# Performance work log

Measured on AMD Instinct MI355X. Metric: run time of the kernel, lower is better.

Reference implementation:

```python
import jax, jax.numpy as jnp
import numpy as np

N, E = 50000, 800000
IN_DIM, HID, HEADS, OUT_DIM = 128, 64, 4, 64
NEG_SLOPE = 0.2


def add_self_loops(edge_index, n):
    loops = jnp.arange(n, dtype=edge_index.dtype)
    return jnp.concatenate([edge_index, jnp.stack([loops, loops])], axis=1)


def gat_layer(x, edge_index, W, att_src, att_dst, bias, heads, ch, concat):
    n = x.shape[0]
    xp = (x @ W).reshape(n, heads, ch)                       # [N,H,C]
    s_src = jnp.sum(xp * att_src, axis=-1)                   # [N,H]
    s_dst = jnp.sum(xp * att_dst, axis=-1)                   # [N,H]
    src, dst = edge_index[0], edge_index[1]
    e = jax.nn.leaky_relu(s_src[src] + s_dst[dst], NEG_SLOPE)  # [E,H]
    # segment softmax over incoming edges of each destination node
    m = jax.ops.segment_max(e, dst, num_segments=n)
    e = jnp.exp(e - m[dst])
    denom = jax.ops.segment_sum(e, dst, num_segments=n)
    alpha = e / (denom[dst] + 1e-16)                         # [E,H]
    out = jax.ops.segment_sum(xp[src] * alpha[:, :, None], dst, num_segments=n)  # [N,H,C]
    out = out.reshape(n, heads * ch) if concat else out.mean(axis=1)
    return out + bias


def setup_inputs() -> dict:
    key = jax.random.key(0)
    ks = jax.random.split(key, 10)
    glorot = lambda k, shape: jax.random.normal(k, shape, jnp.float32) * np.sqrt(2.0 / (shape[0] + shape[-1]))
    return {
        "x": jax.random.normal(ks[0], (N, IN_DIM), jnp.float32),
        "edge_index": jax.random.randint(ks[1], (2, E), 0, N, jnp.int32),
        "W1": glorot(ks[2], (IN_DIM, HEADS * HID)),
        "att_src1": glorot(ks[3], (HEADS, HID)),
        "att_dst1": glorot(ks[4], (HEADS, HID)),
        "bias1": jnp.zeros((HEADS * HID,), jnp.float32),
        "W2": glorot(ks[5], (HEADS * HID, OUT_DIM)),
        "att_src2": glorot(ks[6], (1, OUT_DIM)),
        "att_dst2": glorot(ks[7], (1, OUT_DIM)),
        "bias2": jnp.zeros((OUT_DIM,), jnp.float32),
    }


def reference(x, edge_index, W1, att_src1, att_dst1, bias1, W2, att_src2, att_dst2, bias2):
    ei = add_self_loops(edge_index, x.shape[0])
    h = gat_layer(x, ei, W1, att_src1, att_dst1, bias1, HEADS, HID, concat=True)
    h = jax.nn.relu(h)
    out = gat_layer(h, ei, W2, att_src2, att_dst2, bias2, 1, OUT_DIM, concat=False)
    return out
```

## Files before the change

### kernel.cpp

```cpp
#include <hip/hip_runtime.h>
#include <hip/hip_bf16.h>
#include <hip/hip_fp16.h>

#define NODES 50000
#define NEDGE 800000
#define NE2   850000
#define INDIM 128
#define F1    256
#define HEADS 4
#define HID   64
#define OUTD  64
#define MTILES 3125

#define NB   196
#define PB   196
#define EPB  4096
#define CAP  6144
#define G1B  782

typedef _Float16 f16;
typedef _Float16 f16x8 __attribute__((ext_vector_type(8)));
typedef float    f32x4 __attribute__((ext_vector_type(4)));

__global__ void k_hist(const int* __restrict__ ei, int* __restrict__ blkhist,
                       const float* __restrict__ W1, const float* __restrict__ W2,
                       f16* __restrict__ W1p, f16* __restrict__ W2p)
{
    const int b = blockIdx.x, t = threadIdx.x;
    if (b < PB) {
        __shared__ int h[NB];
        for (int i = t; i < NB; i += 256) h[i] = 0;
        __syncthreads();
        const int e0 = b * EPB;
        const int eend = min(e0 + EPB, NEDGE);
        for (int i = e0 + t; i < eend; i += 256) {
            int d = ei[NEDGE + i];
            atomicAdd(&h[d >> 8], 1);
        }
        __syncthreads();
        for (int i = t; i < NB; i += 256) blkhist[i * PB + b] = h[i];
    } else {
        int idx = (b - PB) * 256 + t;
        if (idx < 32768) {
            int j = idx & 7, l = (idx >> 3) & 63, fi = idx >> 9;
            int kb = fi & 3, ct = fi >> 2;
            int k = kb * 32 + (l >> 4) * 8 + j;
            int col = ct * 16 + (l & 15);
            W1p[idx] = (f16)W1[k * F1 + col];
        } else {
            int i2 = idx - 32768;
            int j = i2 & 7, l = (i2 >> 3) & 63, fi = i2 >> 9;
            int kb = fi & 7, ct = fi >> 3;
            int k = kb * 32 + (l >> 4) * 8 + j;
            int col = ct * 16 + (l & 15);
            W2p[i2] = (f16)W2[k * OUTD + col];
        }
    }
}

__global__ void k_scanR(int* __restrict__ blkhist, int* __restrict__ rowtot)
{
    __shared__ int sh[256];
    const int q = blockIdx.x, t = threadIdx.x;
    int v = (t < PB) ? blkhist[q * PB + t] : 0;
    sh[t] = v; __syncthreads();
    for (int off = 1; off < 256; off <<= 1) {
        int tv = (t >= off) ? sh[t - off] : 0;
        __syncthreads();
        sh[t] += tv;
        __syncthreads();
    }
    if (t < PB) blkhist[q * PB + t] = sh[t] - v;
    if (t == 255) rowtot[q] = sh[255];
}

__global__ void k_part(const int* __restrict__ ei, const int* __restrict__ blkhist,
                       const int* __restrict__ rowtot, unsigned* __restrict__ staged)
{
    const int b = blockIdx.x, t = threadIdx.x;
    __shared__ int sS[256];
    __shared__ int cur[NB];
    int v = (t < NB) ? rowtot[t] : 0;
    sS[t] = v; __syncthreads();
    for (int off = 1; off < 256; off <<= 1) {
        int tv = (t >= off) ? sS[t - off] : 0;
        __syncthreads();
        sS[t] += tv;
        __syncthreads();
    }
    if (t < NB) cur[t] = (sS[t] - v) + blkhist[t * PB + b];
    __syncthreads();
    const int e0 = b * EPB;
    const int eend = min(e0 + EPB, NEDGE);
    for (int i = e0 + t; i < eend; i += 256) {
        int sN = ei[i];
        int d  = ei[NEDGE + i];
        int pos = atomicAdd(&cur[d >> 8], 1);
        staged[pos] = (unsigned)sN | ((unsigned)(d & 255) << 16);
    }
}

__global__ __launch_bounds__(256) void k_bg(
    const unsigned* __restrict__ staged, const int* __restrict__ rowtot,
    int* __restrict__ row_ptr, int* __restrict__ csr_src,
    const float* __restrict__ x, const f16* __restrict__ W1p,
    const float* __restrict__ as1, const float* __restrict__ ad1,
    f16* __restrict__ xp1h, float* __restrict__ ssrc, float* __restrict__ sdst)
{
    if (blockIdx.x < NB) {
        __shared__ unsigned sorted2[CAP];
        __shared__ int bin[256];
        __shared__ int cnt[256];
        __shared__ int sh[256];
        __shared__ int ssum[4];
        const int q = blockIdx.x, t = threadIdx.x;
        const int wv = t >> 6, lane = t & 63;
        int pv = (t < q) ? rowtot[t] : 0;
#pragma unroll
        for (int off = 32; off; off >>= 1) pv += __shfl_xor(pv, off);
        if (lane == 0) ssum[wv] = pv;
        cnt[t] = 0; bin[t] = 0;
        __syncthreads();
        const int estart = ssum[0] + ssum[1] + ssum[2] + ssum[3];
        const int m = rowtot[q];
        const int nodebase = q * 256;
        const int nn = min(256, NODES - nodebase);
        const int csrbase = estart + nodebase;

        const bool dosort = (m <= CAP);
        if (dosort) {
            for (int i = t; i < m; i += 256)
                atomicAdd(&bin[(staged[estart + i] & 0xFFFFu) >> 8], 1);
            __syncthreads();
            int bv = bin[t];
            sh[t] = bv;
            __syncthreads();
            for (int off = 1; off < 256; off <<= 1) {
                int tv = (t >= off) ? sh[t - off] : 0;
                __syncthreads();
                sh[t] += tv;
                __syncthreads();
            }
            bin[t] = sh[t] - bv;
            __syncthreads();
            for (int i = t; i < m; i += 256) {
                unsigned u = staged[estart + i];
                int p = atomicAdd(&bin[(u & 0xFFFFu) >> 8], 1);
                sorted2[p] = u;
            }
            __syncthreads();
        }

        if (dosort) {
            for (int i = t; i < m; i += 256)
                atomicAdd(&cnt[sorted2[i] >> 16], 1);
        } else {
            for (int i = t; i < m; i += 256)
                atomicAdd(&cnt[staged[estart + i] >> 16], 1);
        }
        __syncthreads();
        int v = cnt[t];
        sh[t] = v;
        __syncthreads();
        for (int off = 1; off < 256; off <<= 1) {
            int tv = (t >= off) ? sh[t - off] : 0;
            __syncthreads();
            sh[t] += tv;
            __syncthreads();
        }
        int excl = sh[t] - v;
        __syncthreads();
        if (t < nn) {
            int r = csrbase + excl + t;
            row_ptr[nodebase + t] = r;
            csr_src[r] = nodebase + t;
            cnt[t] = excl + t + 1;
        }
        __syncthreads();
        if (dosort) {
            for (int i = t; i < m; i += 256) {
                unsigned u = sorted2[i];
                int pos = atomicAdd(&cnt[u >> 16], 1);
                csr_src[csrbase + pos] = (int)(u & 0xFFFFu);
            }
        } else {
            for (int i = t; i < m; i += 256) {
                unsigned u = staged[estart + i];
                int pos = atomicAdd(&cnt[u >> 16], 1);
                csr_src[csrbase + pos] = (int)(u & 0xFFFFu);
            }
        }
        if (q == NB - 1 && t == 0) row_ptr[NODES] = NE2;
        return;
    }

    const int wv = threadIdx.x >> 6, lane = threadIdx.x & 63;
    const int l15 = lane & 15, quad = lane >> 4;
    const int rowtile = (blockIdx.x - NB) * 4 + wv;
    if (rowtile >= MTILES) return;
    const int rowbase = rowtile * 16;

    f16x8 afrag[4];
    const float* xrow = x + (rowbase + l15) * INDIM + quad * 8;
#pragma unroll
    for (int kb = 0; kb < 4; ++kb) {
        float4 u0 = *(const float4*)(xrow + kb * 32);
        float4 u1 = *(const float4*)(xrow + kb * 32 + 4);
        f16x8 a;
        a[0] = (f16)u0.x; a[1] = (f16)u0.y; a[2] = (f16)u0.z; a[3] = (f16)u0.w;
        a[4] = (f16)u1.x; a[5] = (f16)u1.y; a[6] = (f16)u1.z; a[7] = (f16)u1.w;
        afrag[kb] = a;
    }

    const f16x8* Wf = (const f16x8*)W1p;
    f32x4 acc[16];
#pragma unroll
    for (int ct = 0; ct < 16; ++ct) acc[ct] = (f32x4){0.f, 0.f, 0.f, 0.f};
#pragma unroll
    for (int ct = 0; ct < 16; ++ct) {
#pragma unroll
        for (int kb = 0; kb < 4; ++kb) {
            f16x8 b = Wf[(ct * 4 + kb) * 64 + lane];
            acc[ct] = __builtin_amdgcn_mfma_f32_16x16x32_f16(afrag[kb], b, acc[ct], 0, 0, 0);
        }
    }
    const int orow = rowbase + quad * 4;
#pragma unroll
    for (int ct = 0; ct < 16; ++ct) {
#pragma unroll
        for (int r = 0; r < 4; ++r)
            xp1h[(orow + r) * F1 + ct * 16 + l15] = (f16)acc[ct][r];
    }
    float ps[4][4], pd[4][4];
#pragma unroll
    for (int h = 0; h < 4; ++h)
#pragma unroll
        for (int r = 0; r < 4; ++r) { ps[h][r] = 0.f; pd[h][r] = 0.f; }
#pragma unroll
    for (int ct = 0; ct < 16; ++ct) {
        float av = as1[ct * 16 + l15];
        float dv = ad1[ct * 16 + l15];
        int h = ct >> 2;
#pragma unroll
        for (int r = 0; r < 4; ++r) {
            ps[h][r] = fmaf(acc[ct][r], av, ps[h][r]);
            pd[h][r] = fmaf(acc[ct][r], dv, pd[h][r]);
        }
    }
#pragma unroll
    for (int off = 8; off; off >>= 1) {
#pragma unroll
        for (int h = 0; h < 4; ++h)
#pragma unroll
            for (int r = 0; r < 4; ++r) {
                ps[h][r] += __shfl_xor(ps[h][r], off);
                pd[h][r] += __shfl_xor(pd[h][r], off);
            }
    }
    if (l15 == 0) {
#pragma unroll
        for (int r = 0; r < 4; ++r) {
            int row = orow + r;
            float4 vs = {ps[0][r], ps[1][r], ps[2][r], ps[3][r]};
            float4 vd = {pd[0][r], pd[1][r], pd[2][r], pd[3][r]};
            ((float4*)ssrc)[row] = vs;
            ((float4*)sdst)[row] = vd;
        }
    }
}

__global__ __launch_bounds__(256) void k_agg1(
    const int* __restrict__ row_ptr, const int* __restrict__ csr_src,
    const float* __restrict__ ssrc, const float* __restrict__ sdst,
    const f16* __restrict__ xp1h, const float* __restrict__ bias,
    f16* __restrict__ hbuf)
{
    const int wv = threadIdx.x >> 6, l = threadIdx.x & 63;
    const int n = blockIdx.x * 4 + wv;
    const int eq = l & 15, ph = l >> 4;
    const int g  = l >> 4, sub = l & 15;
    const int sel_lo = (sub >> 3) << 4;
    const int sel_hi = (2 + (sub >> 3)) << 4;
    const float sd = sdst[n * HEADS + ph];
    const int jbeg = row_ptr[n], jend = row_ptr[n + 1];
    const f16x8* xv = (const f16x8*)xp1h;

    float den = 0.f;
    float alo[8] = {0.f,0.f,0.f,0.f,0.f,0.f,0.f,0.f};
    float ahi[8] = {0.f,0.f,0.f,0.f,0.f,0.f,0.f,0.f};
    for (int base = jbeg; base < jend; base += 16) {
        int c = jend - base; if (c > 16) c = 16;
        int s = 0; float ex = 0.f;
        if (eq < c) {
            s = csr_src[base + eq];
            float e = ssrc[s * HEADS + ph] + sd;
            e = e > 0.f ? e : 0.2f * e;
            ex = __expf(e);
        }
        den += ex;
        int p = 0;
        for (; p + 7 < c; p += 8) {
            int ea = p + g, eb = p + 4 + g;
            int   sa  = __shfl(s, ea),          sb  = __shfl(s, eb);
            float aal = __shfl(ex, ea | sel_lo), aah = __shfl(ex, ea | sel_hi);
            float abl = __shfl(ex, eb | sel_lo), abh = __shfl(ex, eb | sel_hi);
            f16x8 va0 = xv[sa * 32 + sub];
            f16x8 va1 = xv[sa * 32 + sub + 16];
            f16x8 vb0 = xv[sb * 32 + sub];
            f16x8 vb1 = xv[sb * 32 + sub + 16];
#pragma unroll
            for (int j = 0; j < 8; ++j) {
                alo[j] = fmaf(aal, (float)va0[j], alo[j]);
                ahi[j] = fmaf(aah, (float)va1[j], ahi[j]);
            }
#pragma unroll
            for (int j = 0; j < 8; ++j) {
                alo[j] = fmaf(abl, (float)vb0[j], alo[j]);
                ahi[j] = fmaf(abh, (float)vb1[j], ahi[j]);
            }
        }
        for (; p < c; p += 4) {
            int ea = p + g;
            int   sa  = __shfl(s, ea);
            float aal = __shfl(ex, ea | sel_lo), aah = __shfl(ex, ea | sel_hi);
            f16x8 va0 = xv[sa * 32 + sub];
            f16x8 va1 = xv[sa * 32 + sub + 16];
#pragma unroll
            for (int j = 0; j < 8; ++j) {
                alo[j] = fmaf(aal, (float)va0[j], alo[j]);
                ahi[j] = fmaf(aah, (float)va1[j], ahi[j]);
            }
        }
    }
#pragma unroll
    for (int off = 8; off; off >>= 1) den += __shfl_xor(den, off);
    const float dl = __shfl(den, sel_lo);
    const float dh = __shfl(den, sel_hi);
    const float rdl = 1.f / (dl + 1e-16f);
    const float rdh = 1.f / (dh + 1e-16f);
#pragma unroll
    for (int j = 0; j < 8; ++j) {
        alo[j] += __shfl_xor(alo[j], 16); alo[j] += __shfl_xor(alo[j], 32);
        ahi[j] += __shfl_xor(ahi[j], 16); ahi[j] += __shfl_xor(ahi[j], 32);
    }
    if (g == 0) {
        const float4* b4 = (const float4*)bias;
        float4 bl0 = b4[sub * 2],        bl1 = b4[sub * 2 + 1];
        float4 bh0 = b4[(sub + 16) * 2], bh1 = b4[(sub + 16) * 2 + 1];
        f16x8 olo, ohi;
        float v;
        v = fmaf(alo[0], rdl, bl0.x); olo[0] = (f16)(v > 0.f ? v : 0.f);
        v = fmaf(alo[1], rdl, bl0.y); olo[1] = (f16)(v > 0.f ? v : 0.f);
        v = fmaf(alo[2], rdl, bl0.z); olo[2] = (f16)(v > 0.f ? v : 0.f);
        v = fmaf(alo[3], rdl, bl0.w); olo[3] = (f16)(v > 0.f ? v : 0.f);
        v = fmaf(alo[4], rdl, bl1.x); olo[4] = (f16)(v > 0.f ? v : 0.f);
        v = fmaf(alo[5], rdl, bl1.y); olo[5] = (f16)(v > 0.f ? v : 0.f);
        v = fmaf(alo[6], rdl, bl1.z); olo[6] = (f16)(v > 0.f ? v : 0.f);
        v = fmaf(alo[7], rdl, bl1.w); olo[7] = (f16)(v > 0.f ? v : 0.f);
        v = fmaf(ahi[0], rdh, bh0.x); ohi[0] = (f16)(v > 0.f ? v : 0.f);
        v = fmaf(ahi[1], rdh, bh0.y); ohi[1] = (f16)(v > 0.f ? v : 0.f);
        v = fmaf(ahi[2], rdh, bh0.z); ohi[2] = (f16)(v > 0.f ? v : 0.f);
        v = fmaf(ahi[3], rdh, bh0.w); ohi[3] = (f16)(v > 0.f ? v : 0.f);
        v = fmaf(ahi[4], rdh, bh1.x); ohi[4] = (f16)(v > 0.f ? v : 0.f);
        v = fmaf(ahi[5], rdh, bh1.y); ohi[5] = (f16)(v > 0.f ? v : 0.f);
        v = fmaf(ahi[6], rdh, bh1.z); ohi[6] = (f16)(v > 0.f ? v : 0.f);
        v = fmaf(ahi[7], rdh, bh1.w); ohi[7] = (f16)(v > 0.f ? v : 0.f);
        ((f16x8*)hbuf)[n * 32 + sub] = olo;
        ((f16x8*)hbuf)[n * 32 + sub + 16] = ohi;
    }
}

__global__ __launch_bounds__(256) void k_gemm2m(
    const f16* __restrict__ hbuf, const f16* __restrict__ W2p,
    const float* __restrict__ as2, const float* __restrict__ ad2,
    f16* __restrict__ xp2h, float* __restrict__ ssrc, float* __restrict__ sdst)
{
    const int wv = threadIdx.x >> 6, lane = threadIdx.x & 63;
    const int l15 = lane & 15, quad = lane >> 4;
    const int rowtile = blockIdx.x * 4 + wv;
    if (rowtile >= MTILES) return;
    const int rowbase = rowtile * 16;

    const f16x8* Wf = (const f16x8*)W2p;
    f32x4 acc[4];
#pragma unroll
    for (int ct = 0; ct < 4; ++ct) acc[ct] = (f32x4){0.f, 0.f, 0.f, 0.f};
    const f16* hrow = hbuf + (rowbase + l15) * F1 + quad * 8;
#pragma unroll
    for (int kb = 0; kb < 8; ++kb) {
        f16x8 a = *(const f16x8*)(hrow + kb * 32);
#pragma unroll
        for (int ct = 0; ct < 4; ++ct) {
            f16x8 b = Wf[(ct * 8 + kb) * 64 + lane];
            acc[ct] = __builtin_amdgcn_mfma_f32_16x16x32_f16(a, b, acc[ct], 0, 0, 0);
        }
    }
    const int orow = rowbase + quad * 4;
#pragma unroll
    for (int ct = 0; ct < 4; ++ct) {
#pragma unroll
        for (int r = 0; r < 4; ++r)
            xp2h[(orow + r) * OUTD + ct * 16 + l15] = (f16)acc[ct][r];
    }
    float ps[4] = {0.f,0.f,0.f,0.f}, pd[4] = {0.f,0.f,0.f,0.f};
#pragma unroll
    for (int ct = 0; ct < 4; ++ct) {
        float av = as2[ct * 16 + l15];
        float dv = ad2[ct * 16 + l15];
#pragma unroll
        for (int r = 0; r < 4; ++r) {
            ps[r] = fmaf(acc[ct][r], av, ps[r]);
            pd[r] = fmaf(acc[ct][r], dv, pd[r]);
        }
    }
#pragma unroll
    for (int off = 8; off; off >>= 1) {
#pragma unroll
        for (int r = 0; r < 4; ++r) {
            ps[r] += __shfl_xor(ps[r], off);
            pd[r] += __shfl_xor(pd[r], off);
        }
    }
    if (l15 == 0) {
#pragma unroll
        for (int r = 0; r < 4; ++r) {
            ssrc[orow + r] = ps[r];
            sdst[orow + r] = pd[r];
        }
    }
}

__global__ __launch_bounds__(256) void k_agg2(
    const int* __restrict__ row_ptr, const int* __restrict__ csr_src,
    const float* __restrict__ ssrc, const float* __restrict__ sdst,
    const f16* __restrict__ xp2h, const float* __restrict__ bias,
    float* __restrict__ out)
{
    const int wv = threadIdx.x >> 6, l = threadIdx.x & 63;
    const int n = blockIdx.x * 4 + wv;
    const int grp = l >> 3, sub = l & 7;
    const float sd = sdst[n];
    const int jbeg = row_ptr[n], jend = row_ptr[n + 1];
    const f16x8* xv = (const f16x8*)xp2h;

    float den = 0.f;
    float acc[8] = {0.f,0.f,0.f,0.f,0.f,0.f,0.f,0.f};
    for (int base = jbeg; base < jend; base += 64) {
        int c = jend - base; if (c > 64) c = 64;
        int s = 0; float ex = 0.f;
        if (l < c) {
            s = csr_src[base + l];
            float e = ssrc[s] + sd;
            e = e > 0.f ? e : 0.2f * e;
            ex = __expf(e);
        }
        den += ex;
        int i = 0;
        for (; 8 * (i + 1) < c; i += 2) {
            int ea = 8 * i + grp, eb = 8 * i + 8 + grp;
            int   sa = __shfl(s, ea),  sb = __shfl(s, eb);
            float aa = __shfl(ex, ea), ab = __shfl(ex, eb);
            f16x8 va = xv[sa * 8 + sub];
            f16x8 vb = xv[sb * 8 + sub];
#pragma unroll
            for (int j = 0; j < 8; ++j) acc[j] = fmaf(aa, (float)va[j], acc[j]);
#pragma unroll
            for (int j = 0; j < 8; ++j) acc[j] = fmaf(ab, (float)vb[j], acc[j]);
        }
        for (; 8 * i < c; ++i) {
            int eidx = 8 * i + grp;
            int   se = __shfl(s, eidx);
            float ae = __shfl(ex, eidx);
            f16x8 v = xv[se * 8 + sub];
#pragma unroll
            for (int j = 0; j < 8; ++j) acc[j] = fmaf(ae, (float)v[j], acc[j]);
        }
    }
#pragma unroll
    for (int off = 32; off; off >>= 1) den += __shfl_xor(den, off);
    const float rd = 1.f / (den + 1e-16f);
#pragma unroll
    for (int j = 0; j < 8; ++j) {
        acc[j] += __shfl_xor(acc[j], 8);
        acc[j] += __shfl_xor(acc[j], 16);
        acc[j] += __shfl_xor(acc[j], 32);
    }
    if (grp == 0) {
        const float4* b4 = (const float4*)bias;
        float4 ba = b4[sub * 2], bb = b4[sub * 2 + 1];
        float4 o0, o1;
        o0.x = fmaf(acc[0], rd, ba.x); o0.y = fmaf(acc[1], rd, ba.y);
        o0.z = fmaf(acc[2], rd, ba.z); o0.w = fmaf(acc[3], rd, ba.w);
        o1.x = fmaf(acc[4], rd, bb.x); o1.y = fmaf(acc[5], rd, bb.y);
        o1.z = fmaf(acc[6], rd, bb.z); o1.w = fmaf(acc[7], rd, bb.w);
        float4* ov = (float4*)out + n * 16 + sub * 2;
        ov[0] = o0; ov[1] = o1;
    }
}

extern "C" void kernel_launch(void* const* d_in, const int* in_sizes, int n_in,
                              void* d_out, int out_size, void* d_ws, size_t ws_size,
                              hipStream_t stream)
{
    (void)in_sizes; (void)n_in; (void)out_size; (void)ws_size;
    const float* x   = (const float*)d_in[0];
    const int*   ei  = (const int*)d_in[1];
    const float* W1  = (const float*)d_in[2];
    const float* as1 = (const float*)d_in[3];
    const float* ad1 = (const float*)d_in[4];
    const float* b1  = (const float*)d_in[5];
    const float* W2  = (const float*)d_in[6];
    const float* as2 = (const float*)d_in[7];
    const float* ad2 = (const float*)d_in[8];
    const float* b2  = (const float*)d_in[9];
    float* out = (float*)d_out;

    f16* xp1h    = (f16*)d_ws;
    f16* hbuf    = xp1h + (size_t)NODES * F1;
    f16* W1p     = hbuf + (size_t)NODES * F1;
    f16* W2p     = W1p + 32768;
    float* ssrc1 = (float*)(W2p + 16384);
    float* sdst1 = ssrc1 + (size_t)NODES * HEADS;
    float* ssrc2 = sdst1 + (size_t)NODES * HEADS;
    float* sdst2 = ssrc2 + (size_t)NODES;
    int* row_ptr = (int*)(sdst2 + (size_t)NODES);
    int* blkhist = row_ptr + NODES + 1;
    int* rowtot  = blkhist + NB * PB;
    int* csr_src = rowtot + NB;
    unsigned* staged = (unsigned*)(csr_src + NE2);
    f16* xp2h    = xp1h;

    k_hist<<<PB + 192, 256, 0, stream>>>(ei, blkhist, W1, W2, W1p, W2p);
    k_scanR<<<NB, 256, 0, stream>>>(blkhist, rowtot);
    k_part<<<PB, 256, 0, stream>>>(ei, blkhist, rowtot, staged);

    k_bg<<<NB + G1B, 256, 0, stream>>>(staged, rowtot, row_ptr, csr_src,
                                       x, W1p, as1, ad1, xp1h, ssrc1, sdst1);

    k_agg1<<<NODES / 4, 256, 0, stream>>>(row_ptr, csr_src, ssrc1, sdst1,
                                          xp1h, b1, hbuf);

    k_gemm2m<<<(MTILES + 3) / 4, 256, 0, stream>>>(hbuf, W2p, as2, ad2,
                                                   xp2h, ssrc2, sdst2);
    k_agg2<<<NODES / 4, 256, 0, stream>>>(row_ptr, csr_src, ssrc2, sdst2,
                                          xp2h, b2, out);
}
```

Baseline: 228.4 us.

## Fuse layer-2 projection GEMM into layer-1 aggregation kernel via shared memory

```diff
diff --git a/kernel.cpp b/kernel.cpp
--- a/kernel.cpp
+++ b/kernel.cpp
@@ -269,14 +269,21 @@
     }
 }
 
-__global__ __launch_bounds__(256) void k_agg1(
+__global__ __launch_bounds__(512) void k_agg1f(
     const int* __restrict__ row_ptr, const int* __restrict__ csr_src,
     const float* __restrict__ ssrc, const float* __restrict__ sdst,
     const f16* __restrict__ xp1h, const float* __restrict__ bias,
-    f16* __restrict__ hbuf)
-{
-    const int wv = threadIdx.x >> 6, l = threadIdx.x & 63;
-    const int n = blockIdx.x * 4 + wv;
+    const f16* __restrict__ W2p, const float* __restrict__ as2,
+    const float* __restrict__ ad2,
+    f16* __restrict__ xp2h, float* __restrict__ ssrc2, float* __restrict__ sdst2)
+{
+    __shared__ f16 hl[16][256];
+    f16x8* hu = (f16x8*)&hl[0][0];
+    const int t = threadIdx.x;
+    if (t < 256) hu[256 + t] = (f16x8){0,0,0,0,0,0,0,0};
+
+    const int wv = t >> 6, l = t & 63;
+    const int n = blockIdx.x * 8 + wv;
     const int eq = l & 15, ph = l >> 4;
     const int g  = l >> 4, sub = l & 15;
     const int sel_lo = (sub >> 3) << 4;
@@ -365,67 +372,65 @@
         v = fmaf(ahi[5], rdh, bh1.y); ohi[5] = (f16)(v > 0.f ? v : 0.f);
         v = fmaf(ahi[6], rdh, bh1.z); ohi[6] = (f16)(v > 0.f ? v : 0.f);
         v = fmaf(ahi[7], rdh, bh1.w); ohi[7] = (f16)(v > 0.f ? v : 0.f);
-        ((f16x8*)hbuf)[n * 32 + sub] = olo;
-        ((f16x8*)hbuf)[n * 32 + sub + 16] = ohi;
-    }
-}
-
-__global__ __launch_bounds__(256) void k_gemm2m(
-    const f16* __restrict__ hbuf, const f16* __restrict__ W2p,
-    const float* __restrict__ as2, const float* __restrict__ ad2,
-    f16* __restrict__ xp2h, float* __restrict__ ssrc, float* __restrict__ sdst)
-{
-    const int wv = threadIdx.x >> 6, lane = threadIdx.x & 63;
-    const int l15 = lane & 15, quad = lane >> 4;
-    const int rowtile = blockIdx.x * 4 + wv;
-    if (rowtile >= MTILES) return;
-    const int rowbase = rowtile * 16;
-
-    const f16x8* Wf = (const f16x8*)W2p;
-    f32x4 acc[4];
-#pragma unroll
-    for (int ct = 0; ct < 4; ++ct) acc[ct] = (f32x4){0.f, 0.f, 0.f, 0.f};
-    const f16* hrow = hbuf + (rowbase + l15) * F1 + quad * 8;
-#pragma unroll
-    for (int kb = 0; kb < 8; ++kb) {
-        f16x8 a = *(const f16x8*)(hrow + kb * 32);
+        hu[wv * 32 + sub]      = olo;
+        hu[wv * 32 + sub + 16] = ohi;
+    }
+    __syncthreads();
+
+    if (wv == 0) {
+        const int lane = l;
+        const int l15 = lane & 15, quad = lane >> 4;
+        const f16x8* Wf = (const f16x8*)W2p;
+        f32x4 acc2[4];
+#pragma unroll
+        for (int ct = 0; ct < 4; ++ct) acc2[ct] = (f32x4){0.f, 0.f, 0.f, 0.f};
+#pragma unroll
+        for (int kb = 0; kb < 8; ++kb) {
+            f16x8 a = hu[l15 * 32 + quad + kb * 4];
+#pragma unroll
+            for (int ct = 0; ct < 4; ++ct) {
+                f16x8 b = Wf[(ct * 8 + kb) * 64 + lane];
+                acc2[ct] = __builtin_amdgcn_mfma_f32_16x16x32_f16(a, b, acc2[ct], 0, 0, 0);
+            }
+        }
+        const int rowbase = blockIdx.x * 8;
 #pragma unroll
         for (int ct = 0; ct < 4; ++ct) {
-            f16x8 b = Wf[(ct * 8 + kb) * 64 + lane];
-            acc[ct] = __builtin_amdgcn_mfma_f32_16x16x32_f16(a, b, acc[ct], 0, 0, 0);
-        }
-    }
-    const int orow = rowbase + quad * 4;
-#pragma unroll
-    for (int ct = 0; ct < 4; ++ct) {
-#pragma unroll
-        for (int r = 0; r < 4; ++r)
-            xp2h[(orow + r) * OUTD + ct * 16 + l15] = (f16)acc[ct][r];
-    }
-    float ps[4] = {0.f,0.f,0.f,0.f}, pd[4] = {0.f,0.f,0.f,0.f};
-#pragma unroll
-    for (int ct = 0; ct < 4; ++ct) {
-        float av = as2[ct * 16 + l15];
-        float dv = ad2[ct * 16 + l15];
-#pragma unroll
-        for (int r = 0; r < 4; ++r) {
-            ps[r] = fmaf(acc[ct][r], av, ps[r]);
-            pd[r] = fmaf(acc[ct][r], dv, pd[r]);
-        }
-    }
-#pragma unroll
-    for (int off = 8; off; off >>= 1) {
-#pragma unroll
-        for (int r = 0; r < 4; ++r) {
-            ps[r] += __shfl_xor(ps[r], off);
-            pd[r] += __shfl_xor(pd[r], off);
-        }
-    }
-    if (l15 == 0) {
-#pragma unroll
-        for (int r = 0; r < 4; ++r) {
-            ssrc[orow + r] = ps[r];
-            sdst[orow + r] = pd[r];
+#pragma unroll
+            for (int r = 0; r < 4; ++r) {
+                int row = quad * 4 + r;
+                if (row < 8)
+                    xp2h[(rowbase + row) * OUTD + ct * 16 + l15] = (f16)acc2[ct][r];
+            }
+        }
+        float ps[4] = {0.f,0.f,0.f,0.f}, pd[4] = {0.f,0.f,0.f,0.f};
+#pragma unroll
+        for (int ct = 0; ct < 4; ++ct) {
+            float av = as2[ct * 16 + l15];
+            float dv = ad2[ct * 16 + l15];
+#pragma unroll
+            for (int r = 0; r < 4; ++r) {
+                ps[r] = fmaf(acc2[ct][r], av, ps[r]);
+                pd[r] = fmaf(acc2[ct][r], dv, pd[r]);
+            }
+        }
+#pragma unroll
+        for (int off = 8; off; off >>= 1) {
+#pragma unroll
+            for (int r = 0; r < 4; ++r) {
+                ps[r] += __shfl_xor(ps[r], off);
+                pd[r] += __shfl_xor(pd[r], off);
+            }
+        }
+        if (l15 == 0) {
+#pragma unroll
+            for (int r = 0; r < 4; ++r) {
+                int row = quad * 4 + r;
+                if (row < 8) {
+                    ssrc2[rowbase + row] = ps[r];
+                    sdst2[rowbase + row] = pd[r];
+                }
+            }
         }
     }
 }
@@ -516,8 +521,8 @@
     float* out = (float*)d_out;
 
     f16* xp1h    = (f16*)d_ws;
-    f16* hbuf    = xp1h + (size_t)NODES * F1;
-    f16* W1p     = hbuf + (size_t)NODES * F1;
+    f16* xp2h    = xp1h + (size_t)NODES * F1;
+    f16* W1p     = xp2h + (size_t)NODES * OUTD;
     f16* W2p     = W1p + 32768;
     float* ssrc1 = (float*)(W2p + 16384);
     float* sdst1 = ssrc1 + (size_t)NODES * HEADS;
@@ -528,7 +533,6 @@
     int* rowtot  = blkhist + NB * PB;
     int* csr_src = rowtot + NB;
     unsigned* staged = (unsigned*)(csr_src + NE2);
-    f16* xp2h    = xp1h;
 
     k_hist<<<PB + 192, 256, 0, stream>>>(ei, blkhist, W1, W2, W1p, W2p);
     k_scanR<<<NB, 256, 0, stream>>>(blkhist, rowtot);
@@ -537,11 +541,10 @@
     k_bg<<<NB + G1B, 256, 0, stream>>>(staged, rowtot, row_ptr, csr_src,
                                        x, W1p, as1, ad1, xp1h, ssrc1, sdst1);
 
-    k_agg1<<<NODES / 4, 256, 0, stream>>>(row_ptr, csr_src, ssrc1, sdst1,
-                                          xp1h, b1, hbuf);
-
-    k_gemm2m<<<(MTILES + 3) / 4, 256, 0, stream>>>(hbuf, W2p, as2, ad2,
-                                                   xp2h, ssrc2, sdst2);
+    k_agg1f<<<NODES / 8, 512, 0, stream>>>(row_ptr, csr_src, ssrc1, sdst1,
+                                           xp1h, b1, W2p, as2, ad2,
+                                           xp2h, ssrc2, sdst2);
+
     k_agg2<<<NODES / 4, 256, 0, stream>>>(row_ptr, csr_src, ssrc2, sdst2,
                                           xp2h, b2, out);
 }
```

Result: no change. 227.4 us (-0.5%).
